# Kernel tuning notes

Measured on AMD Instinct MI355X. Metric: run time of the kernel, lower is better.

The kernel has to match this reference:

```python
import jax, jax.numpy as jnp
import numpy as np

B, N, H, D = 8, 2048, 8, 64  # batch, seq, heads, head_dim
DM = H * D                   # model dim = 512


def setup_inputs() -> dict:
    key = jax.random.key(0)
    ks = jax.random.split(key, 9)
    std = 0.02
    return {
        "x": jax.random.normal(ks[0], (B, N, DM), dtype=jnp.float32),
        "Wq": jax.random.normal(ks[1], (H, D, D), dtype=jnp.float32) * std,
        "bq": jnp.zeros((H, D), dtype=jnp.float32),
        "Wk": jax.random.normal(ks[2], (H, D, D), dtype=jnp.float32) * std,
        "bk": jnp.zeros((H, D), dtype=jnp.float32),
        "Wv": jax.random.normal(ks[3], (H, D, D), dtype=jnp.float32) * std,
        "bv": jnp.zeros((H, D), dtype=jnp.float32),
        "Wp": jax.random.normal(ks[4], (DM, DM), dtype=jnp.float32) * std,
        "bp": jnp.zeros((DM,), dtype=jnp.float32),
    }


def reference(x, Wq, bq, Wk, bk, Wv, bv, Wp, bp):
    b, n, dm = x.shape
    # rearrange 'b n (h d) -> b h n d'
    xh = x.reshape(b, n, H, D).transpose(0, 2, 1, 3)  # [b,h,n,d]
    # per-head linear projections (torch Linear: y = x W^T + b), batched over heads
    q = jnp.einsum('bhnd,hed->bhne', xh, Wq) + bq[None, :, None, :]
    k = jnp.einsum('bhnd,hed->bhne', xh, Wk) + bk[None, :, None, :]
    v = jnp.einsum('bhnd,hed->bhne', xh, Wv) + bv[None, :, None, :]
    scale = 1.0 / jnp.sqrt(jnp.asarray(D, dtype=x.dtype))
    scores = jnp.einsum('bhqe,bhke->bhqk', q, k) * scale  # [b,h,n,n]
    attn = jax.nn.softmax(scores, axis=-1)
    out = jnp.einsum('bhqk,bhke->bhqe', attn, v)          # [b,h,n,d]
    # 'b h n d -> b n (h d)' then output projection
    out = out.transpose(0, 2, 1, 3).reshape(b, n, H * D)
    return out @ Wp.T + bp
```

## Files before the change

kernel.cpp:

```cpp
#include <hip/hip_runtime.h>
#include <hip/hip_bf16.h>

#define B_ 8
#define N_ 2048
#define H_ 8
#define DM_ 512
#define NT_ 32
#define NTH_ 16

typedef __bf16 bf16x8 __attribute__((ext_vector_type(8)));
typedef float f32x4 __attribute__((ext_vector_type(4)));
typedef float f32x16 __attribute__((ext_vector_type(16)));
typedef unsigned short us8 __attribute__((ext_vector_type(8)));
typedef unsigned short us4 __attribute__((ext_vector_type(4)));
typedef unsigned int u32x4 __attribute__((ext_vector_type(4)));

#define QSCALE 0.1803368801111204f

__device__ __forceinline__ int swz(int row, int byte_in_row) {
  return row * 128 + (byte_in_row ^ ((row & 7) << 4));
}

__device__ __forceinline__ unsigned short f2bf(float x) {
  __bf16 h = (__bf16)x;
  return __builtin_bit_cast(unsigned short, h);
}

__device__ __forceinline__ float fexp2(float x) {
#if __has_builtin(__builtin_amdgcn_exp2f)
  return __builtin_amdgcn_exp2f(x);
#else
  return exp2f(x);
#endif
}

__device__ __forceinline__ unsigned cvtpk(float a, float b) {
  unsigned r;
  asm("v_cvt_pk_bf16_f32 %0, %1, %2" : "=v"(r) : "v"(a), "v"(b));
  return r;
}

__device__ __forceinline__ void plswap(unsigned& a, unsigned& b) {
#if __has_builtin(__builtin_amdgcn_permlane32_swap)
  auto r = __builtin_amdgcn_permlane32_swap(a, b, false, false);
  a = r[0];
  b = r[1];
#else
  asm("v_permlane32_swap_b32 %0, %1" : "+v"(a), "+v"(b));
#endif
}

__device__ __forceinline__ f32x4 mfma16(bf16x8 a, bf16x8 b, f32x4 c) {
  return __builtin_amdgcn_mfma_f32_16x16x32_bf16(a, b, c, 0, 0, 0);
}
__device__ __forceinline__ f32x16 mfma32(bf16x8 a, bf16x8 b, f32x16 c) {
  return __builtin_amdgcn_mfma_f32_32x32x16_bf16(a, b, c, 0, 0, 0);
}

__device__ __forceinline__ bf16x8 ldg8(const unsigned short* p) {
  return *reinterpret_cast<const bf16x8*>(p);
}

__device__ __forceinline__ void stage_f32_tile(const float* __restrict__ src,
                                               int src_stride, char* dst, int t) {
#pragma unroll
  for (int rep = 0; rep < 4; ++rep) {
    int cid = rep * 256 + t;
    int row = cid >> 4, c4 = cid & 15;
    float4 v = *reinterpret_cast<const float4*>(src + (size_t)row * src_stride + c4 * 4);
    us4 o;
    o[0] = f2bf(v.x); o[1] = f2bf(v.y); o[2] = f2bf(v.z); o[3] = f2bf(v.w);
    *reinterpret_cast<us4*>(dst + row * 128 + ((c4 * 8) ^ ((row & 7) << 4))) = o;
  }
}

__device__ __forceinline__ void stage_bf16_tile(const unsigned short* __restrict__ src,
                                                int src_stride, char* dst, int t) {
#pragma unroll
  for (int rep = 0; rep < 2; ++rep) {
    int cid = rep * 256 + t;
    int row = cid >> 3, c = cid & 7;
    us8 v = *reinterpret_cast<const us8*>(src + (size_t)row * src_stride + c * 8);
    *reinterpret_cast<us8*>(dst + row * 128 + ((c * 16) ^ ((row & 7) << 4))) = v;
  }
}

__global__ __launch_bounds__(256, 4) void qkv_kernel(
    const float* __restrict__ x,
    const float* __restrict__ Wq, const float* __restrict__ bq,
    const float* __restrict__ Wk, const float* __restrict__ bk,
    const float* __restrict__ Wv, const float* __restrict__ bv,
    unsigned short* __restrict__ Qf, unsigned short* __restrict__ Kf,
    unsigned short* __restrict__ Vf) {
  __shared__ __align__(16) char sX[8192];
  __shared__ __align__(16) char sWq[8192];
  __shared__ __align__(16) char sWk[8192];
  __shared__ __align__(16) char sWv[8192];

  const int t = threadIdx.x;
  const int bh = blockIdx.y, h = bh & 7, b = bh >> 3;
  const int n0 = blockIdx.x * 64;
  const int lane = t & 63, w = t >> 6, g = lane >> 4, li = lane & 15;

  stage_f32_tile(x + ((size_t)(b * N_ + n0)) * DM_ + h * 64, DM_, sX, t);
  stage_f32_tile(Wq + (size_t)h * 4096, 64, sWq, t);
  stage_f32_tile(Wk + (size_t)h * 4096, 64, sWk, t);
  stage_f32_tile(Wv + (size_t)h * 4096, 64, sWv, t);
  __syncthreads();

  bf16x8 xa0 = *reinterpret_cast<const bf16x8*>(sX + swz(16 * w + li, 16 * g));
  bf16x8 xa1 = *reinterpret_cast<const bf16x8*>(sX + swz(16 * w + li, 64 + 16 * g));

  const size_t seg = (size_t)N_ * 64;
  const int qkbase =
      ((n0 >> 5) + (w >> 1)) * 2048 + (li >> 3) * 256 + (w & 1) * 128 + (li & 7);
  const int vbase =
      (n0 >> 6) * 4096 + w * 512 + (g >> 1) * 256 + 4 * (g & 1) + li * 8;

  unsigned short* Qs = Qf + (size_t)bh * seg;
  unsigned short* Ks = Kf + (size_t)bh * seg;
  unsigned short* Vs = Vf + (size_t)bh * seg;

#pragma unroll
  for (int c = 0; c < 4; ++c) {
    f32x4 a = {0.f, 0.f, 0.f, 0.f};
    bf16x8 b0 = *reinterpret_cast<const bf16x8*>(sWq + swz(c * 16 + li, 16 * g));
    bf16x8 b1 = *reinterpret_cast<const bf16x8*>(sWq + swz(c * 16 + li, 64 + 16 * g));
    a = mfma16(xa0, b0, a);
    a = mfma16(xa1, b1, a);
    float bb = bq[h * 64 + c * 16 + li];
#pragma unroll
    for (int i = 0; i < 4; ++i)
      Qs[qkbase + c * 512 + (4 * g + i) * 8] = f2bf((a[i] + bb) * QSCALE);
  }
#pragma unroll
  for (int c = 0; c < 4; ++c) {
    f32x4 a = {0.f, 0.f, 0.f, 0.f};
    bf16x8 b0 = *reinterpret_cast<const bf16x8*>(sWk + swz(c * 16 + li, 16 * g));
    bf16x8 b1 = *reinterpret_cast<const bf16x8*>(sWk + swz(c * 16 + li, 64 + 16 * g));
    a = mfma16(xa0, b0, a);
    a = mfma16(xa1, b1, a);
    float bb = bk[h * 64 + c * 16 + li];
#pragma unroll
    for (int i = 0; i < 4; ++i)
      Ks[qkbase + c * 512 + (4 * g + i) * 8] = f2bf(a[i] + bb);
  }
#pragma unroll
  for (int c = 0; c < 4; ++c) {
    f32x4 a = {0.f, 0.f, 0.f, 0.f};
    bf16x8 b0 = *reinterpret_cast<const bf16x8*>(sWv + swz(c * 16 + li, 16 * g));
    bf16x8 b1 = *reinterpret_cast<const bf16x8*>(sWv + swz(c * 16 + li, 64 + 16 * g));
    a = mfma16(xa0, b0, a);
    a = mfma16(xa1, b1, a);
    float bb = bv[h * 64 + c * 16 + li];
    us4 pk;
#pragma unroll
    for (int i = 0; i < 4; ++i) pk[i] = f2bf(a[i] + bb);
    *reinterpret_cast<us4*>(Vs + vbase + (c >> 1) * 2048 + (c & 1) * 128) = pk;
  }
}

__global__ __launch_bounds__(256, 3) void attn_kernel(
    const unsigned short* __restrict__ Qf, const unsigned short* __restrict__ Kf,
    const unsigned short* __restrict__ Vf, unsigned short* __restrict__ AOw) {
  __shared__ float mo[32][2][64];
  __shared__ float ml[2][64];

  const int t = threadIdx.x;
  const int lane = t & 63, w = t >> 6;
  const int lo = lane & 31;
  const int qhalf = w & 1, khalf = w >> 1;

  const int bid = blockIdx.x;
  const int work = (bid & 7) * 256 + (bid >> 3);
  const int bh = work >> 5;
  const int qc = work & 31;
  const int qb = qc * 2 + qhalf;
  const int h = bh & 7, b = bh >> 3;

  const size_t seg = (size_t)N_ * 64;
  const unsigned short* qp = Qf + (size_t)bh * seg + qb * 2048 + lane * 8;
  const unsigned short* kp = Kf + (size_t)bh * seg + (size_t)khalf * NTH_ * 4096 + lane * 8;
  const unsigned short* vp = Vf + (size_t)bh * seg + (size_t)khalf * NTH_ * 4096 + lane * 8;

  bf16x8 qf[4];
#pragma unroll
  for (int dd = 0; dd < 4; ++dd) qf[dd] = ldg8(qp + dd * 512);

  bf16x8 kf[8], vf[8];
#pragma unroll
  for (int j = 0; j < 8; ++j) kf[j] = ldg8(kp + j * 512);

  f32x16 o0 = {}, o1 = {};
  float l = 0.f;

#pragma unroll 1
  for (int kt = 0; kt < NTH_; ++kt) {
    {
      const unsigned short* vpt = vp + (size_t)kt * 4096;
#pragma unroll
      for (int j = 0; j < 8; ++j) vf[j] = ldg8(vpt + j * 512);
    }
    __builtin_amdgcn_sched_barrier(0);

    f32x16 s0 = {}, s1 = {};
    __builtin_amdgcn_s_setprio(1);
#pragma unroll
    for (int dd = 0; dd < 4; ++dd) {
      s0 = mfma32(kf[dd], qf[dd], s0);
      s1 = mfma32(kf[4 + dd], qf[dd], s1);
    }
    __builtin_amdgcn_s_setprio(0);

    if (kt + 1 < NTH_) {
      const unsigned short* kpt = kp + (size_t)(kt + 1) * 4096;
#pragma unroll
      for (int j = 0; j < 8; ++j) kf[j] = ldg8(kpt + j * 512);
    }
    __builtin_amdgcn_sched_barrier(0);

    float ts0 = 0.f, ts1 = 0.f, ts2 = 0.f, ts3 = 0.f;
#pragma unroll
    for (int r = 0; r < 16; r += 4) {
      s0[r + 0] = fexp2(s0[r + 0]); ts0 += s0[r + 0];
      s0[r + 1] = fexp2(s0[r + 1]); ts1 += s0[r + 1];
      s0[r + 2] = fexp2(s0[r + 2]); ts2 += s0[r + 2];
      s0[r + 3] = fexp2(s0[r + 3]); ts3 += s0[r + 3];
      s1[r + 0] = fexp2(s1[r + 0]); ts0 += s1[r + 0];
      s1[r + 1] = fexp2(s1[r + 1]); ts1 += s1[r + 1];
      s1[r + 2] = fexp2(s1[r + 2]); ts2 += s1[r + 2];
      s1[r + 3] = fexp2(s1[r + 3]); ts3 += s1[r + 3];
    }
    l += (ts0 + ts1) + (ts2 + ts3);

    unsigned pl0[4], ph0[4], pl1[4], ph1[4];
#pragma unroll
    for (int qi = 0; qi < 4; ++qi) {
      pl0[qi] = cvtpk(s0[4 * qi + 0], s0[4 * qi + 1]);
      ph0[qi] = cvtpk(s0[4 * qi + 2], s0[4 * qi + 3]);
      pl1[qi] = cvtpk(s1[4 * qi + 0], s1[4 * qi + 1]);
      ph1[qi] = cvtpk(s1[4 * qi + 2], s1[4 * qi + 3]);
    }
    plswap(pl0[0], pl0[1]); plswap(ph0[0], ph0[1]);
    plswap(pl0[2], pl0[3]); plswap(ph0[2], ph0[3]);
    plswap(pl1[0], pl1[1]); plswap(ph1[0], ph1[1]);
    plswap(pl1[2], pl1[3]); plswap(ph1[2], ph1[3]);
    bf16x8 pf0, pf1, pf2, pf3;
    {
      u32x4 w0 = {pl0[0], ph0[0], pl0[1], ph0[1]};
      u32x4 w1 = {pl0[2], ph0[2], pl0[3], ph0[3]};
      u32x4 w2 = {pl1[0], ph1[0], pl1[1], ph1[1]};
      u32x4 w3 = {pl1[2], ph1[2], pl1[3], ph1[3]};
      pf0 = __builtin_bit_cast(bf16x8, w0);
      pf1 = __builtin_bit_cast(bf16x8, w1);
      pf2 = __builtin_bit_cast(bf16x8, w2);
      pf3 = __builtin_bit_cast(bf16x8, w3);
    }

    __builtin_amdgcn_s_setprio(1);
    o0 = mfma32(vf[0], pf0, o0);
    o1 = mfma32(vf[4], pf0, o1);
    o0 = mfma32(vf[1], pf1, o0);
    o1 = mfma32(vf[5], pf1, o1);
    o0 = mfma32(vf[2], pf2, o0);
    o1 = mfma32(vf[6], pf2, o1);
    o0 = mfma32(vf[3], pf3, o0);
    o1 = mfma32(vf[7], pf3, o1);
    __builtin_amdgcn_s_setprio(0);
  }

  if (khalf) {
#pragma unroll
    for (int j = 0; j < 16; ++j) {
      mo[j][qhalf][lane] = o0[j];
      mo[16 + j][qhalf][lane] = o1[j];
    }
    ml[qhalf][lane] = l;
  }
  __syncthreads();
  if (khalf) return;

#pragma unroll
  for (int j = 0; j < 16; ++j) {
    o0[j] += mo[j][qhalf][lane];
    o1[j] += mo[16 + j][qhalf][lane];
  }
  l += ml[qhalf][lane];

  l += __shfl_xor(l, 32);
  const int hi = lane >> 5;
  const float invl = 1.0f / l;
  unsigned short* aoptr =
      AOw + ((size_t)(b * N_) + qb * 32 + lo) * DM_ + h * 64 + 4 * hi;
#pragma unroll
  for (int qi = 0; qi < 4; ++qi) {
    us4 pk;
#pragma unroll
    for (int rr = 0; rr < 4; ++rr) pk[rr] = f2bf(o0[4 * qi + rr] * invl);
    *reinterpret_cast<us4*>(aoptr + 8 * qi) = pk;
  }
#pragma unroll
  for (int qi = 0; qi < 4; ++qi) {
    us4 pk;
#pragma unroll
    for (int rr = 0; rr < 4; ++rr) pk[rr] = f2bf(o1[4 * qi + rr] * invl);
    *reinterpret_cast<us4*>(aoptr + 32 + 8 * qi) = pk;
  }
}

__global__ __launch_bounds__(256, 4) void proj_kernel(
    const unsigned short* __restrict__ AOw, const float* __restrict__ Wp,
    const float* __restrict__ bp, float* __restrict__ out) {
  __shared__ __align__(16) char sA[8192];
  __shared__ __align__(16) char sB[8192];

  const int t = threadIdx.x;
  const int r0 = blockIdx.x * 64;
  const int i0 = blockIdx.y * 64;
  const int lane = t & 63, w = t >> 6, g = lane >> 4, li = lane & 15;

  f32x4 acc[4];
#pragma unroll
  for (int c = 0; c < 4; ++c) {
    acc[c][0] = 0.f; acc[c][1] = 0.f; acc[c][2] = 0.f; acc[c][3] = 0.f;
  }

  for (int jt = 0; jt < 8; ++jt) {
    __syncthreads();
    stage_bf16_tile(AOw + (size_t)r0 * DM_ + jt * 64, DM_, sA, t);
    stage_f32_tile(Wp + (size_t)i0 * DM_ + jt * 64, DM_, sB, t);
    __syncthreads();

    bf16x8 a0 = *reinterpret_cast<const bf16x8*>(sA + swz(16 * w + li, 16 * g));
    bf16x8 a1 = *reinterpret_cast<const bf16x8*>(sA + swz(16 * w + li, 64 + 16 * g));
#pragma unroll
    for (int c = 0; c < 4; ++c) {
      bf16x8 b0 = *reinterpret_cast<const bf16x8*>(sB + swz(c * 16 + li, 16 * g));
      bf16x8 b1 = *reinterpret_cast<const bf16x8*>(sB + swz(c * 16 + li, 64 + 16 * g));
      acc[c] = mfma16(a0, b0, acc[c]);
      acc[c] = mfma16(a1, b1, acc[c]);
    }
  }

#pragma unroll
  for (int c = 0; c < 4; ++c) {
    float bb = bp[i0 + c * 16 + li];
#pragma unroll
    for (int i = 0; i < 4; ++i)
      out[(size_t)(r0 + 16 * w + 4 * g + i) * DM_ + i0 + c * 16 + li] = acc[c][i] + bb;
  }
}

extern "C" void kernel_launch(void* const* d_in, const int* in_sizes, int n_in,
                              void* d_out, int out_size, void* d_ws, size_t ws_size,
                              hipStream_t stream) {
  const float* x  = (const float*)d_in[0];
  const float* Wq = (const float*)d_in[1];
  const float* bq = (const float*)d_in[2];
  const float* Wk = (const float*)d_in[3];
  const float* bk = (const float*)d_in[4];
  const float* Wv = (const float*)d_in[5];
  const float* bv = (const float*)d_in[6];
  const float* Wp = (const float*)d_in[7];
  const float* bp = (const float*)d_in[8];
  float* out = (float*)d_out;

  const size_t seg = (size_t)B_ * H_ * N_ * 64;
  unsigned short* Qf  = (unsigned short*)d_ws;
  unsigned short* Kf  = Qf + seg;
  unsigned short* Vf  = Kf + seg;
  unsigned short* AOw = Vf + seg;

  qkv_kernel<<<dim3(32, 64), 256, 0, stream>>>(x, Wq, bq, Wk, bk, Wv, bv, Qf, Kf, Vf);
  attn_kernel<<<dim3(2048), 256, 0, stream>>>(Qf, Kf, Vf, AOw);
  proj_kernel<<<dim3(256, 8), 256, 0, stream>>>(AOw, Wp, bp, out);
}
```

Measured before the change: 136.8 us.

## Compute softmax row sums via MFMA with ones and prefetch V one tile ahead

Replaces the VALU accumulation of the softmax denominator with an extra MFMA that multiplies a ones vector by the P fragments. The row sum then comes out already reduced across lanes, so the cross-half shuffle is dropped. V loads move to after the PV MFMAs to prefetch the next tile, giving them a full iteration of latency hiding. The occupancy hint rises from 3 to 4 waves per SIMD. These changes add an MFMA-issue cost and a 16-register accumulator, and the tighter register budget could cause spills.

```diff
diff --git a/kernel.cpp b/kernel.cpp
--- a/kernel.cpp
+++ b/kernel.cpp
@@ -160,7 +160,7 @@
   }
 }
 
-__global__ __launch_bounds__(256, 3) void attn_kernel(
+__global__ __launch_bounds__(256, 4) void attn_kernel(
     const unsigned short* __restrict__ Qf, const unsigned short* __restrict__ Kf,
     const unsigned short* __restrict__ Vf, unsigned short* __restrict__ AOw) {
   __shared__ float mo[32][2][64];
@@ -183,6 +183,10 @@
   const unsigned short* kp = Kf + (size_t)bh * seg + (size_t)khalf * NTH_ * 4096 + lane * 8;
   const unsigned short* vp = Vf + (size_t)bh * seg + (size_t)khalf * NTH_ * 4096 + lane * 8;
 
+  const unsigned one2 = 0x3F803F80u;
+  u32x4 onesw = {one2, one2, one2, one2};
+  const bf16x8 ones8 = __builtin_bit_cast(bf16x8, onesw);
+
   bf16x8 qf[4];
 #pragma unroll
   for (int dd = 0; dd < 4; ++dd) qf[dd] = ldg8(qp + dd * 512);
@@ -190,19 +194,13 @@
   bf16x8 kf[8], vf[8];
 #pragma unroll
   for (int j = 0; j < 8; ++j) kf[j] = ldg8(kp + j * 512);
-
-  f32x16 o0 = {}, o1 = {};
-  float l = 0.f;
+#pragma unroll
+  for (int j = 0; j < 8; ++j) vf[j] = ldg8(vp + j * 512);
+
+  f32x16 o0 = {}, o1 = {}, lacc = {};
 
 #pragma unroll 1
   for (int kt = 0; kt < NTH_; ++kt) {
-    {
-      const unsigned short* vpt = vp + (size_t)kt * 4096;
-#pragma unroll
-      for (int j = 0; j < 8; ++j) vf[j] = ldg8(vpt + j * 512);
-    }
-    __builtin_amdgcn_sched_barrier(0);
-
     f32x16 s0 = {}, s1 = {};
     __builtin_amdgcn_s_setprio(1);
 #pragma unroll
@@ -219,19 +217,11 @@
     }
     __builtin_amdgcn_sched_barrier(0);
 
-    float ts0 = 0.f, ts1 = 0.f, ts2 = 0.f, ts3 = 0.f;
-#pragma unroll
-    for (int r = 0; r < 16; r += 4) {
-      s0[r + 0] = fexp2(s0[r + 0]); ts0 += s0[r + 0];
-      s0[r + 1] = fexp2(s0[r + 1]); ts1 += s0[r + 1];
-      s0[r + 2] = fexp2(s0[r + 2]); ts2 += s0[r + 2];
-      s0[r + 3] = fexp2(s0[r + 3]); ts3 += s0[r + 3];
-      s1[r + 0] = fexp2(s1[r + 0]); ts0 += s1[r + 0];
-      s1[r + 1] = fexp2(s1[r + 1]); ts1 += s1[r + 1];
-      s1[r + 2] = fexp2(s1[r + 2]); ts2 += s1[r + 2];
-      s1[r + 3] = fexp2(s1[r + 3]); ts3 += s1[r + 3];
-    }
-    l += (ts0 + ts1) + (ts2 + ts3);
+#pragma unroll
+    for (int r = 0; r < 16; ++r) {
+      s0[r] = fexp2(s0[r]);
+      s1[r] = fexp2(s1[r]);
+    }
 
     unsigned pl0[4], ph0[4], pl1[4], ph1[4];
 #pragma unroll
@@ -260,13 +250,24 @@
     __builtin_amdgcn_s_setprio(1);
     o0 = mfma32(vf[0], pf0, o0);
     o1 = mfma32(vf[4], pf0, o1);
+    lacc = mfma32(ones8, pf0, lacc);
     o0 = mfma32(vf[1], pf1, o0);
     o1 = mfma32(vf[5], pf1, o1);
+    lacc = mfma32(ones8, pf1, lacc);
     o0 = mfma32(vf[2], pf2, o0);
     o1 = mfma32(vf[6], pf2, o1);
+    lacc = mfma32(ones8, pf2, lacc);
     o0 = mfma32(vf[3], pf3, o0);
     o1 = mfma32(vf[7], pf3, o1);
+    lacc = mfma32(ones8, pf3, lacc);
     __builtin_amdgcn_s_setprio(0);
+
+    if (kt + 1 < NTH_) {
+      const unsigned short* vpt = vp + (size_t)(kt + 1) * 4096;
+#pragma unroll
+      for (int j = 0; j < 8; ++j) vf[j] = ldg8(vpt + j * 512);
+    }
+    __builtin_amdgcn_sched_barrier(0);
   }
 
   if (khalf) {
@@ -275,7 +276,7 @@
       mo[j][qhalf][lane] = o0[j];
       mo[16 + j][qhalf][lane] = o1[j];
     }
-    ml[qhalf][lane] = l;
+    ml[qhalf][lane] = lacc[0];
   }
   __syncthreads();
   if (khalf) return;
@@ -285,9 +286,8 @@
     o0[j] += mo[j][qhalf][lane];
     o1[j] += mo[16 + j][qhalf][lane];
   }
-  l += ml[qhalf][lane];
-
-  l += __shfl_xor(l, 32);
+  const float l = lacc[0] + ml[qhalf][lane];
+
   const int hi = lane >> 5;
   const float invl = 1.0f / l;
   unsigned short* aoptr =
```

Result: slower. 448.1 us (+227.5%).
